# Optimization experiments

Measured on AMD Instinct MI355X. Metric: run time of the kernel, lower is better.

## Reference

```python
import jax, jax.numpy as jnp
import numpy as np

H = 1024        # hidden_size
NH = 16         # num_attention_heads
HD = H // NH    # attention_head_size = 64
EPS = 1e-12


def setup_inputs() -> dict:
    key = jax.random.key(0)
    ks = jax.random.split(key, 12)
    B, S = 2, 2048
    s = 0.02
    return {
        "hidden_states": jax.random.normal(ks[0], (B, S, H), jnp.float32),
        "attention_mask": jnp.zeros((B, 1, 1, S), jnp.float32),
        "Wq": jax.random.normal(ks[1], (H, H), jnp.float32) * s,
        "bq": jnp.zeros((H,), jnp.float32),
        "Wk": jax.random.normal(ks[2], (H, H), jnp.float32) * s,
        "bk": jnp.zeros((H,), jnp.float32),
        "Wv": jax.random.normal(ks[3], (H, H), jnp.float32) * s,
        "bv": jnp.zeros((H,), jnp.float32),
        "Wd": jax.random.normal(ks[4], (H, H), jnp.float32) * s,
        "bd": jnp.zeros((H,), jnp.float32),
        "ln_gamma": jnp.ones((H,), jnp.float32),
        "ln_beta": jnp.zeros((H,), jnp.float32),
    }


def _split_heads(x):
    # [B,S,H] -> [B,NH,S,HD]
    B, S, _ = x.shape
    return x.reshape(B, S, NH, HD).transpose(0, 2, 1, 3)


def reference(hidden_states, attention_mask, Wq, bq, Wk, bk, Wv, bv, Wd, bd, ln_gamma, ln_beta):
    q = _split_heads(hidden_states @ Wq.T + bq)
    k = _split_heads(hidden_states @ Wk.T + bk)
    v = _split_heads(hidden_states @ Wv.T + bv)

    scores = jnp.einsum("bhqd,bhkd->bhqk", q, k) / jnp.sqrt(jnp.float32(HD))
    scores = scores + attention_mask
    probs = jax.nn.softmax(scores, axis=-1)  # attention dropout p=0

    ctx = jnp.einsum("bhqk,bhkd->bhqd", probs, v)
    B, _, S, _ = ctx.shape
    ctx = ctx.transpose(0, 2, 1, 3).reshape(B, S, H)

    proj = ctx @ Wd.T + bd  # output dropout p=0
    x = hidden_states + proj
    mu = jnp.mean(x, axis=-1, keepdims=True)
    var = jnp.mean(jnp.square(x - mu), axis=-1, keepdims=True)
    out = (x - mu) * jax.lax.rsqrt(var + EPS) * ln_gamma + ln_beta
    return out
```

## Files before the change

kernel.cpp:

```cpp
#include <hip/hip_runtime.h>

typedef unsigned short u16;
typedef __attribute__((ext_vector_type(4))) unsigned short u16x4;
typedef __attribute__((ext_vector_type(8))) unsigned short u16x8;
typedef __attribute__((ext_vector_type(8))) __bf16 bf16x8;
typedef __attribute__((ext_vector_type(4))) float f32x4;

#define S_LEN 2048
#define HDIM 1024
#define NHEAD 16
#define HD 64
#define MTOK 4096
#define QKV_STRIDE 4194304
#define LOG2E 1.44269504089f
#define QKSCL (0.125f * 1.44269504089f)

__device__ __forceinline__ float bf2f(u16 h) {
    unsigned u = ((unsigned)h) << 16;
    return __builtin_bit_cast(float, u);
}
__device__ __forceinline__ u16 f2bf(float f) {
    return __builtin_bit_cast(u16, (__bf16)f);
}
__device__ __forceinline__ bf16x8 as_bf16(u16x8 u) {
    union { u16x8 a; bf16x8 b; } c; c.a = u; return c.b;
}
__device__ __forceinline__ void gld_lds16(const u16* g, u16* l) {
    __builtin_amdgcn_global_load_lds((const __attribute__((address_space(1))) u16*)g,
                                     (__attribute__((address_space(3))) u16*)l, 16, 0, 0);
}

__device__ __forceinline__ void cast4(const float* __restrict__ s, u16* __restrict__ d, int i) {
    f32x4 v = *(const f32x4*)(s + (size_t)i * 4);
    u16x4 o;
    o[0] = f2bf(v[0]); o[1] = f2bf(v[1]); o[2] = f2bf(v[2]); o[3] = f2bf(v[3]);
    *(u16x4*)(d + (size_t)i * 4) = o;
}

__global__ __launch_bounds__(256) void prep(const float* __restrict__ hs,
                                            const float* __restrict__ Wq, const float* __restrict__ Wk,
                                            const float* __restrict__ Wv, const float* __restrict__ Wd,
                                            const float* __restrict__ bq, const float* __restrict__ bk,
                                            const float* __restrict__ bv,
                                            u16* __restrict__ hsb, u16* __restrict__ wqkvb,
                                            u16* __restrict__ wdb, float* __restrict__ b3) {
    int bid = blockIdx.x, tid = threadIdx.x;
    if (bid < 4096) {
        cast4(hs, hsb, bid * 256 + tid);
    } else if (bid < 5120) {
        cast4(Wq, wqkvb, (bid - 4096) * 256 + tid);
    } else if (bid < 6144) {
        cast4(Wk, wqkvb + HDIM * HDIM, (bid - 5120) * 256 + tid);
    } else if (bid < 7168) {
        cast4(Wv, wqkvb + 2 * HDIM * HDIM, (bid - 6144) * 256 + tid);
    } else if (bid < 8192) {
        cast4(Wd, wdb, (bid - 7168) * 256 + tid);
    } else {
        int i = (bid - 8192) * 256 + tid;
        if (i < 3072) b3[i] = (i < 1024) ? bq[i] : (i < 2048) ? bk[i - 1024] : bv[i - 2048];
    }
}

template <int MODE>
__global__ __launch_bounds__(256, 3) void gemm_bt(const u16* __restrict__ A, const u16* __restrict__ Bw,
                                                  const float* __restrict__ bias,
                                                  u16* __restrict__ outb, u16* __restrict__ vtout,
                                                  float* __restrict__ outf,
                                                  int Md, int Nd, int Kd) {
    __shared__ alignas(16) u16 As[2][128 * 32];
    __shared__ alignas(16) u16 Bs[2][128 * 32];
    const int tid = threadIdx.x;
    const int wave = tid >> 6, lane = tid & 63;
    const int l15 = lane & 15, l4 = lane >> 4;
    const int m0 = blockIdx.y * 128, n0 = blockIdx.x * 128;
    const int wm = wave >> 1, wn = wave & 1;

    const int cc0 = wave * 2;
    const int srow = lane >> 2;
    const int sco = (lane & 3) * 8;

    f32x4 acc[4][4];
#pragma unroll
    for (int i = 0; i < 4; i++)
#pragma unroll
        for (int j = 0; j < 4; j++) acc[i][j] = (f32x4){0.f, 0.f, 0.f, 0.f};

    auto STAGE = [&](int k0, int buf) {
#pragma unroll
        for (int i = 0; i < 2; i++) {
            int cc = cc0 + i;
            int row = cc * 16 + srow;
            gld_lds16(A + (size_t)(m0 + row) * Kd + k0 + sco, &As[buf][cc * 512]);
            gld_lds16(Bw + (size_t)(n0 + row) * Kd + k0 + sco, &Bs[buf][cc * 512]);
        }
    };

    const int nt = Kd >> 5;
    STAGE(0, 0);
    for (int t = 0; t < nt; ++t) {
        __builtin_amdgcn_s_barrier();
        if (t + 1 < nt) {
            STAGE((t + 1) << 5, (t + 1) & 1);
            asm volatile("s_waitcnt vmcnt(4)" ::: "memory");
        } else {
            asm volatile("s_waitcnt vmcnt(0)" ::: "memory");
        }
        __builtin_amdgcn_s_barrier();
        const u16* as = &As[t & 1][0];
        const u16* bs = &Bs[t & 1][0];
        bf16x8 af[4], bf[4];
#pragma unroll
        for (int x = 0; x < 4; x++) {
            af[x] = as_bf16(*(const u16x8*)&as[(wm * 64 + x * 16 + l15) * 32 + l4 * 8]);
            bf[x] = as_bf16(*(const u16x8*)&bs[(wn * 64 + x * 16 + l15) * 32 + l4 * 8]);
        }
        __builtin_amdgcn_s_setprio(1);
#pragma unroll
        for (int mi = 0; mi < 4; mi++)
#pragma unroll
            for (int nj = 0; nj < 4; nj++)
                acc[mi][nj] = __builtin_amdgcn_mfma_f32_16x16x32_bf16(af[mi], bf[nj], acc[mi][nj], 0, 0, 0);
        __builtin_amdgcn_s_setprio(0);
    }

#pragma unroll
    for (int mi = 0; mi < 4; mi++) {
#pragma unroll
        for (int nj = 0; nj < 4; nj++) {
            int coln = n0 + wn * 64 + nj * 16 + l15;
            float bv_ = bias[coln];
            int rowb = m0 + wm * 64 + mi * 16 + l4 * 4;
            if (MODE == 0) {
                int which = coln >> 10, nn = coln & 1023;
                int hh = nn >> 6, dd = nn & 63;
                int bb = rowb >> 11, ss = rowb & 2047;
                if (which < 2) {
#pragma unroll
                    for (int r = 0; r < 4; r++)
                        outb[(size_t)which * QKV_STRIDE + ((size_t)((bb << 4) + hh) * S_LEN + ss + r) * HD + dd] =
                            f2bf(acc[mi][nj][r] + bv_);
                } else {
                    u16x4 o;
#pragma unroll
                    for (int r = 0; r < 4; r++) o[r] = f2bf(acc[mi][nj][r] + bv_);
                    *(u16x4*)(vtout + ((size_t)((bb << 4) + hh) * HD + dd) * S_LEN + ss) = o;
                }
            } else {
#pragma unroll
                for (int r = 0; r < 4; r++)
                    outf[(size_t)(rowb + r) * Nd + coln] = acc[mi][nj][r] + bv_;
            }
        }
    }
}

__global__ __launch_bounds__(512, 6) void flash_attn5(const u16* __restrict__ qkv,
                                                      const u16* __restrict__ vt,
                                                      const float* __restrict__ amask,
                                                      u16* __restrict__ ctx) {
    __shared__ alignas(16) u16 Kb[2][4096];
    __shared__ alignas(16) u16 Vb[2][4096];
    __shared__ alignas(16) u16 Pl[8][1024];
    __shared__ u16 Mlb[2048];

    const int tid = threadIdx.x;
    const int wave = tid >> 6, lane = tid & 63;
    const int l15 = lane & 15, l4 = lane >> 4;
    const int lid = blockIdx.x;
    const int idx = lid >> 3;
    const int bh = (lid & 7) * 4 + (idx >> 4);
    const int qx = idx & 15;
    const int b = bh >> 4, h = bh & 15;
    const int qr0 = qx * 128 + wave * 16;

    const u16* qh = qkv + (size_t)bh * (S_LEN * HD);
    const u16* kh = qh + QKV_STRIDE;
    const u16* vth = vt + (size_t)bh * (S_LEN * HD);
    u16* pw = &Pl[wave][0];

    {
        f32x4 m = *(const f32x4*)(amask + (size_t)b * S_LEN + tid * 4);
        u16x4 mm;
#pragma unroll
        for (int j = 0; j < 4; j++) mm[j] = f2bf(m[j] * LOG2E);
        *(u16x4*)&Mlb[tid * 4] = mm;
    }

    bf16x8 qf[2];
#pragma unroll
    for (int ks = 0; ks < 2; ks++)
        qf[ks] = as_bf16(*(const u16x8*)(qh + (size_t)(qr0 + l15) * HD + ks * 32 + l4 * 8));

    __syncthreads();

    const int srow = lane >> 3;
    const int schunk = (lane & 7) ^ srow;
    const int krow = wave * 8 + srow;
    const u16* ksrc = kh + (size_t)krow * HD + schunk * 8;
    const u16* vsrc = vth + (size_t)krow * S_LEN + schunk * 8;

    f32x4 acc_o[4];
    float l_run = 0.f;
#pragma unroll
    for (int x = 0; x < 4; x++) acc_o[x] = (f32x4){0.f, 0.f, 0.f, 0.f};

    auto STAGE = [&](int T, int buf) {
        gld_lds16(ksrc + (size_t)T * 64 * HD, &Kb[buf][wave * 512]);
        gld_lds16(vsrc + T * 64, &Vb[buf][wave * 512]);
    };

    auto tile = [&](int t, int buf) {
        const u16* kb = &Kb[buf][0];
        const u16* vb = &Vb[buf][0];
        f32x4 accs[4];
#pragma unroll
        for (int nj = 0; nj < 4; nj++) accs[nj] = (f32x4){0.f, 0.f, 0.f, 0.f};
        __builtin_amdgcn_s_setprio(1);
#pragma unroll
        for (int ks = 0; ks < 2; ks++) {
            bf16x8 kf[4];
#pragma unroll
            for (int nj = 0; nj < 4; nj++) {
                int n = nj * 16 + l15;
                kf[nj] = as_bf16(*(const u16x8*)&kb[n * 64 + ((ks * 32 + l4 * 8) ^ ((n & 7) << 3))]);
            }
#pragma unroll
            for (int nj = 0; nj < 4; nj++)
                accs[nj] = __builtin_amdgcn_mfma_f32_16x16x32_bf16(kf[nj], qf[ks], accs[nj], 0, 0, 0);
        }
        __builtin_amdgcn_s_setprio(0);
        const int kv0 = t * 64;
        const int rsw = (l15 & 7) << 3;
#pragma unroll
        for (int nj = 0; nj < 4; nj++) {
            u16x4 mraw = *(const u16x4*)&Mlb[kv0 + nj * 16 + l4 * 4];
            u16x4 o;
#pragma unroll
            for (int r = 0; r < 4; r++) {
                float p = __builtin_amdgcn_exp2f(accs[nj][r] * QKSCL + bf2f(mraw[r]));
                l_run += p;
                o[r] = f2bf(p);
            }
            *(u16x4*)&pw[l15 * 64 + ((nj * 16 + l4 * 4) ^ rsw)] = o;
        }
        __builtin_amdgcn_s_setprio(1);
#pragma unroll
        for (int ks = 0; ks < 2; ks++) {
            int kvoff = ks * 32 + l4 * 8;
            bf16x8 pf = as_bf16(*(const u16x8*)&pw[l15 * 64 + (kvoff ^ rsw)]);
            bf16x8 vf[4];
#pragma unroll
            for (int dj = 0; dj < 4; dj++) {
                int d = dj * 16 + l15;
                vf[dj] = as_bf16(*(const u16x8*)&vb[d * 64 + (kvoff ^ ((d & 7) << 3))]);
            }
#pragma unroll
            for (int dj = 0; dj < 4; dj++)
                acc_o[dj] = __builtin_amdgcn_mfma_f32_16x16x32_bf16(vf[dj], pf, acc_o[dj], 0, 0, 0);
        }
        __builtin_amdgcn_s_setprio(0);
    };

    STAGE(0, 0);
    for (int t = 0; t < 32; ++t) {
        __builtin_amdgcn_s_barrier();
        if (t + 1 < 32) {
            STAGE(t + 1, (t + 1) & 1);
            asm volatile("s_waitcnt vmcnt(2)" ::: "memory");
        } else {
            asm volatile("s_waitcnt vmcnt(0)" ::: "memory");
        }
        __builtin_amdgcn_s_barrier();
        tile(t, t & 1);
    }

    float l = l_run;
    l += __shfl_xor(l, 16);
    l += __shfl_xor(l, 32);
    float inv = 1.0f / l;
    u16* cp = ctx + ((size_t)b * S_LEN + qr0 + l15) * HDIM + h * HD + l4 * 4;
#pragma unroll
    for (int dj = 0; dj < 4; dj++) {
        u16x4 o;
#pragma unroll
        for (int r = 0; r < 4; r++) o[r] = f2bf(acc_o[dj][r] * inv);
        *(u16x4*)(cp + dj * 16) = o;
    }
}

__global__ __launch_bounds__(256) void resid_ln(const float* __restrict__ hs, const float* __restrict__ proj,
                                                const float* __restrict__ g, const float* __restrict__ be,
                                                float* __restrict__ out) {
    int row = blockIdx.x, tid = threadIdx.x;
    int base = row * HDIM + tid * 4;
    f32x4 a = *(const f32x4*)(hs + base);
    f32x4 p = *(const f32x4*)(proj + base);
    f32x4 x = a + p;
    float s = x[0] + x[1] + x[2] + x[3];
    float sq = x[0] * x[0] + x[1] * x[1] + x[2] * x[2] + x[3] * x[3];
#pragma unroll
    for (int m = 1; m < 64; m <<= 1) {
        s += __shfl_xor(s, m);
        sq += __shfl_xor(sq, m);
    }
    __shared__ float red[8];
    int wave = tid >> 6, lane = tid & 63;
    if (lane == 0) { red[wave] = s; red[4 + wave] = sq; }
    __syncthreads();
    s = red[0] + red[1] + red[2] + red[3];
    sq = red[4] + red[5] + red[6] + red[7];
    float mean = s * (1.0f / 1024.0f);
    float var = sq * (1.0f / 1024.0f) - mean * mean;
    float rstd = rsqrtf(fmaxf(var, 0.f) + 1e-12f);
    f32x4 gg = *(const f32x4*)(g + tid * 4);
    f32x4 bb = *(const f32x4*)(be + tid * 4);
    f32x4 o;
#pragma unroll
    for (int j = 0; j < 4; j++) o[j] = (x[j] - mean) * rstd * gg[j] + bb[j];
    *(f32x4*)(out + base) = o;
}

extern "C" void kernel_launch(void* const* d_in, const int* in_sizes, int n_in,
                              void* d_out, int out_size, void* d_ws, size_t ws_size,
                              hipStream_t stream) {
    const float* hs    = (const float*)d_in[0];
    const float* amask = (const float*)d_in[1];
    const float* Wq    = (const float*)d_in[2];
    const float* bq    = (const float*)d_in[3];
    const float* Wk    = (const float*)d_in[4];
    const float* bk    = (const float*)d_in[5];
    const float* Wv    = (const float*)d_in[6];
    const float* bv    = (const float*)d_in[7];
    const float* Wd    = (const float*)d_in[8];
    const float* bd    = (const float*)d_in[9];
    const float* gamma = (const float*)d_in[10];
    const float* beta  = (const float*)d_in[11];

    char* ws = (char*)d_ws;
    u16*   hsb   = (u16*)(ws);
    u16*   Wqkvb = (u16*)(ws + ((size_t)8 << 20));
    u16*   Wdb   = (u16*)(ws + ((size_t)14 << 20));
    u16*   qkv   = (u16*)(ws + ((size_t)16 << 20));
    u16*   vt    = qkv + 2 * (size_t)QKV_STRIDE;
    u16*   ctx   = (u16*)(ws + ((size_t)40 << 20));
    float* proj  = (float*)(ws + ((size_t)48 << 20));
    float* b3    = (float*)(ws + ((size_t)64 << 20));

    prep<<<8204, 256, 0, stream>>>(hs, Wq, Wk, Wv, Wd, bq, bk, bv, hsb, Wqkvb, Wdb, b3);

    gemm_bt<0><<<dim3(24, 32), 256, 0, stream>>>(hsb, Wqkvb, b3, qkv, vt, nullptr, MTOK, 3072, HDIM);

    flash_attn5<<<512, 512, 0, stream>>>(qkv, vt, amask, ctx);

    gemm_bt<1><<<dim3(8, 32), 256, 0, stream>>>(ctx, Wdb, bd, nullptr, nullptr, proj, MTOK, HDIM, HDIM);

    resid_ln<<<MTOK, 256, 0, stream>>>(hs, proj, gamma, beta, (float*)d_out);
}
```

Baseline: 128.4 us.

## Rework attention with 32x32 MFMA, in-register P via permlane, split-KV wave groups

The flash attention kernel switches from 16x16x32 to 32x32x16 bf16 MFMAs, with each wave handling 32 query rows. The probability tile now stays in registers: a permlane32 swap rearranges it into the B-operand layout instead of a round trip through LDS. The 8 waves form two groups that process alternating KV tiles, and their partial outputs and row sums are combined through shared memory at the end. The mask is kept in fp32, and the occupancy hint drops from 6 to 4 in exchange for larger register tiles and 72KB of LDS.

```diff
diff --git a/kernel.cpp b/kernel.cpp
--- a/kernel.cpp
+++ b/kernel.cpp
@@ -1,10 +1,13 @@
 #include <hip/hip_runtime.h>
 
 typedef unsigned short u16;
+typedef unsigned int u32;
 typedef __attribute__((ext_vector_type(4))) unsigned short u16x4;
 typedef __attribute__((ext_vector_type(8))) unsigned short u16x8;
 typedef __attribute__((ext_vector_type(8))) __bf16 bf16x8;
 typedef __attribute__((ext_vector_type(4))) float f32x4;
+typedef __attribute__((ext_vector_type(16))) float f32x16;
+typedef __attribute__((ext_vector_type(2))) int i32x2;
 
 #define S_LEN 2048
 #define HDIM 1024
@@ -28,6 +31,20 @@
 __device__ __forceinline__ void gld_lds16(const u16* g, u16* l) {
     __builtin_amdgcn_global_load_lds((const __attribute__((address_space(1))) u16*)g,
                                      (__attribute__((address_space(3))) u16*)l, 16, 0, 0);
+}
+
+__device__ __forceinline__ void pl32swap(u32& a, u32& b) {
+#if __has_builtin(__builtin_amdgcn_permlane32_swap)
+    i32x2 r = __builtin_amdgcn_permlane32_swap((int)a, (int)b, false, false);
+    a = (u32)r[0]; b = (u32)r[1];
+#else
+    u32 as = (u32)__shfl_xor((int)a, 32);
+    u32 bs = (u32)__shfl_xor((int)b, 32);
+    bool hi = (threadIdx.x & 32) != 0;
+    u32 na = hi ? bs : a;
+    u32 nb = hi ? b : as;
+    a = na; b = nb;
+#endif
 }
 
 __device__ __forceinline__ void cast4(const float* __restrict__ s, u16* __restrict__ d, int i) {
@@ -154,119 +171,133 @@
     }
 }
 
-__global__ __launch_bounds__(512, 6) void flash_attn5(const u16* __restrict__ qkv,
+__global__ __launch_bounds__(512, 4) void flash_attn6(const u16* __restrict__ qkv,
                                                       const u16* __restrict__ vt,
                                                       const float* __restrict__ amask,
                                                       u16* __restrict__ ctx) {
-    __shared__ alignas(16) u16 Kb[2][4096];
-    __shared__ alignas(16) u16 Vb[2][4096];
-    __shared__ alignas(16) u16 Pl[8][1024];
-    __shared__ u16 Mlb[2048];
+    __shared__ alignas(16) char smem[73728];
 
     const int tid = threadIdx.x;
     const int wave = tid >> 6, lane = tid & 63;
-    const int l15 = lane & 15, l4 = lane >> 4;
+    const int l31 = lane & 31;
+    const int hi = lane >> 5;
+    const int hi4 = hi * 4;
+    const int ws = wave & 3;
+    const int g = wave >> 2;
+
     const int lid = blockIdx.x;
     const int idx = lid >> 3;
     const int bh = (lid & 7) * 4 + (idx >> 4);
     const int qx = idx & 15;
     const int b = bh >> 4, h = bh & 15;
-    const int qr0 = qx * 128 + wave * 16;
+    const int qr0 = qx * 128 + ws * 32;
 
     const u16* qh = qkv + (size_t)bh * (S_LEN * HD);
     const u16* kh = qh + QKV_STRIDE;
     const u16* vth = vt + (size_t)bh * (S_LEN * HD);
-    u16* pw = &Pl[wave][0];
+
+    u16* kbase = (u16*)(smem + g * 32768);
+    u16* vbase = kbase + 8192;
+    float* Ml = (float*)(smem + 65536);
 
     {
         f32x4 m = *(const f32x4*)(amask + (size_t)b * S_LEN + tid * 4);
-        u16x4 mm;
-#pragma unroll
-        for (int j = 0; j < 4; j++) mm[j] = f2bf(m[j] * LOG2E);
-        *(u16x4*)&Mlb[tid * 4] = mm;
-    }
-
-    bf16x8 qf[2];
-#pragma unroll
-    for (int ks = 0; ks < 2; ks++)
-        qf[ks] = as_bf16(*(const u16x8*)(qh + (size_t)(qr0 + l15) * HD + ks * 32 + l4 * 8));
+#pragma unroll
+        for (int j = 0; j < 4; j++) m[j] *= LOG2E;
+        *(f32x4*)&Ml[tid * 4] = m;
+    }
+
+    bf16x8 qf[4];
+#pragma unroll
+    for (int s = 0; s < 4; ++s)
+        qf[s] = as_bf16(*(const u16x8*)(qh + (size_t)(qr0 + l31) * HD + s * 16 + hi * 8));
 
     __syncthreads();
 
     const int srow = lane >> 3;
     const int schunk = (lane & 7) ^ srow;
-    const int krow = wave * 8 + srow;
-    const u16* ksrc = kh + (size_t)krow * HD + schunk * 8;
-    const u16* vsrc = vth + (size_t)krow * S_LEN + schunk * 8;
-
-    f32x4 acc_o[4];
+    const u16* kss = kh + (size_t)(ws * 16 + srow) * HD + schunk * 8;
+    const u16* vss = vth + (size_t)(ws * 16 + srow) * S_LEN + schunk * 8;
+
+    f32x16 oacc[2];
+#pragma unroll
+    for (int d = 0; d < 2; ++d)
+#pragma unroll
+        for (int i = 0; i < 16; ++i) oacc[d][i] = 0.f;
     float l_run = 0.f;
-#pragma unroll
-    for (int x = 0; x < 4; x++) acc_o[x] = (f32x4){0.f, 0.f, 0.f, 0.f};
-
-    auto STAGE = [&](int T, int buf) {
-        gld_lds16(ksrc + (size_t)T * 64 * HD, &Kb[buf][wave * 512]);
-        gld_lds16(vsrc + T * 64, &Vb[buf][wave * 512]);
+
+    auto STAGE = [&](int tloc, int buf) {
+        const int kv0 = ((tloc << 1) + g) << 6;
+        const u16* ks = kss + (size_t)kv0 * HD;
+        const u16* vs = vss + kv0;
+        u16* kd = kbase + buf * 4096 + ws * 1024;
+        u16* vd = vbase + buf * 4096 + ws * 1024;
+        gld_lds16(ks, kd);
+        gld_lds16(ks + 8 * HD, kd + 512);
+        gld_lds16(vs, vd);
+        gld_lds16(vs + 8 * S_LEN, vd + 512);
     };
 
-    auto tile = [&](int t, int buf) {
-        const u16* kb = &Kb[buf][0];
-        const u16* vb = &Vb[buf][0];
-        f32x4 accs[4];
-#pragma unroll
-        for (int nj = 0; nj < 4; nj++) accs[nj] = (f32x4){0.f, 0.f, 0.f, 0.f};
-        __builtin_amdgcn_s_setprio(1);
-#pragma unroll
-        for (int ks = 0; ks < 2; ks++) {
-            bf16x8 kf[4];
-#pragma unroll
-            for (int nj = 0; nj < 4; nj++) {
-                int n = nj * 16 + l15;
-                kf[nj] = as_bf16(*(const u16x8*)&kb[n * 64 + ((ks * 32 + l4 * 8) ^ ((n & 7) << 3))]);
+    auto tile = [&](int tloc, int buf) {
+        const int kv0 = ((tloc << 1) + g) << 6;
+        const u16* kb = kbase + buf * 4096;
+        const u16* vb = vbase + buf * 4096;
+#pragma unroll
+        for (int sub = 0; sub < 2; ++sub) {
+            f32x16 accs;
+#pragma unroll
+            for (int i = 0; i < 16; ++i) accs[i] = 0.f;
+            const int kvrow = sub * 32 + l31;
+            const int ksw = (kvrow & 7) << 3;
+            __builtin_amdgcn_s_setprio(1);
+#pragma unroll
+            for (int s = 0; s < 4; ++s) {
+                bf16x8 kf = as_bf16(*(const u16x8*)&kb[kvrow * 64 + (((s * 2 + hi) << 3) ^ ksw)]);
+                accs = __builtin_amdgcn_mfma_f32_32x32x16_bf16(kf, qf[s], accs, 0, 0, 0);
             }
-#pragma unroll
-            for (int nj = 0; nj < 4; nj++)
-                accs[nj] = __builtin_amdgcn_mfma_f32_16x16x32_bf16(kf[nj], qf[ks], accs[nj], 0, 0, 0);
-        }
-        __builtin_amdgcn_s_setprio(0);
-        const int kv0 = t * 64;
-        const int rsw = (l15 & 7) << 3;
-#pragma unroll
-        for (int nj = 0; nj < 4; nj++) {
-            u16x4 mraw = *(const u16x4*)&Mlb[kv0 + nj * 16 + l4 * 4];
-            u16x4 o;
-#pragma unroll
-            for (int r = 0; r < 4; r++) {
-                float p = __builtin_amdgcn_exp2f(accs[nj][r] * QKSCL + bf2f(mraw[r]));
-                l_run += p;
-                o[r] = f2bf(p);
+            __builtin_amdgcn_s_setprio(0);
+            u32 pw_[8];
+#pragma unroll
+            for (int rg = 0; rg < 4; ++rg) {
+                f32x4 mk = *(const f32x4*)&Ml[kv0 + sub * 32 + rg * 8 + hi4];
+#pragma unroll
+                for (int r2 = 0; r2 < 2; ++r2) {
+                    float pa = __builtin_amdgcn_exp2f(accs[rg * 4 + r2 * 2] * QKSCL + mk[r2 * 2]);
+                    float pb = __builtin_amdgcn_exp2f(accs[rg * 4 + r2 * 2 + 1] * QKSCL + mk[r2 * 2 + 1]);
+                    l_run += pa + pb;
+                    pw_[rg * 2 + r2] = (u32)f2bf(pa) | ((u32)f2bf(pb) << 16);
+                }
             }
-            *(u16x4*)&pw[l15 * 64 + ((nj * 16 + l4 * 4) ^ rsw)] = o;
-        }
-        __builtin_amdgcn_s_setprio(1);
-#pragma unroll
-        for (int ks = 0; ks < 2; ks++) {
-            int kvoff = ks * 32 + l4 * 8;
-            bf16x8 pf = as_bf16(*(const u16x8*)&pw[l15 * 64 + (kvoff ^ rsw)]);
-            bf16x8 vf[4];
-#pragma unroll
-            for (int dj = 0; dj < 4; dj++) {
-                int d = dj * 16 + l15;
-                vf[dj] = as_bf16(*(const u16x8*)&vb[d * 64 + (kvoff ^ ((d & 7) << 3))]);
+            pl32swap(pw_[0], pw_[2]);
+            pl32swap(pw_[1], pw_[3]);
+            pl32swap(pw_[4], pw_[6]);
+            pl32swap(pw_[5], pw_[7]);
+            union { u32 w[4]; u16x8 v; } f0, f1;
+            f0.w[0] = pw_[0]; f0.w[1] = pw_[1]; f0.w[2] = pw_[2]; f0.w[3] = pw_[3];
+            f1.w[0] = pw_[4]; f1.w[1] = pw_[5]; f1.w[2] = pw_[6]; f1.w[3] = pw_[7];
+            bf16x8 pf0 = as_bf16(f0.v), pf1 = as_bf16(f1.v);
+            __builtin_amdgcn_s_setprio(1);
+#pragma unroll
+            for (int dsub = 0; dsub < 2; ++dsub) {
+                const int drow = dsub * 32 + l31;
+                const int dsw = (drow & 7) << 3;
+                const int c0 = (sub * 4 + hi) << 3;
+                const int c1 = ((sub * 2 + 1) * 2 + hi) << 3;
+                bf16x8 vf0 = as_bf16(*(const u16x8*)&vb[drow * 64 + (c0 ^ dsw)]);
+                oacc[dsub] = __builtin_amdgcn_mfma_f32_32x32x16_bf16(vf0, pf0, oacc[dsub], 0, 0, 0);
+                bf16x8 vf1 = as_bf16(*(const u16x8*)&vb[drow * 64 + (c1 ^ dsw)]);
+                oacc[dsub] = __builtin_amdgcn_mfma_f32_32x32x16_bf16(vf1, pf1, oacc[dsub], 0, 0, 0);
             }
-#pragma unroll
-            for (int dj = 0; dj < 4; dj++)
-                acc_o[dj] = __builtin_amdgcn_mfma_f32_16x16x32_bf16(vf[dj], pf, acc_o[dj], 0, 0, 0);
-        }
-        __builtin_amdgcn_s_setprio(0);
+            __builtin_amdgcn_s_setprio(0);
+        }
     };
 
     STAGE(0, 0);
-    for (int t = 0; t < 32; ++t) {
+    for (int t = 0; t < 16; ++t) {
         __builtin_amdgcn_s_barrier();
-        if (t + 1 < 32) {
+        if (t + 1 < 16) {
             STAGE(t + 1, (t + 1) & 1);
-            asm volatile("s_waitcnt vmcnt(2)" ::: "memory");
+            asm volatile("s_waitcnt vmcnt(4)" ::: "memory");
         } else {
             asm volatile("s_waitcnt vmcnt(0)" ::: "memory");
         }
@@ -274,17 +305,40 @@
         tile(t, t & 1);
     }
 
-    float l = l_run;
-    l += __shfl_xor(l, 16);
-    l += __shfl_xor(l, 32);
-    float inv = 1.0f / l;
-    u16* cp = ctx + ((size_t)b * S_LEN + qr0 + l15) * HDIM + h * HD + l4 * 4;
-#pragma unroll
-    for (int dj = 0; dj < 4; dj++) {
-        u16x4 o;
-#pragma unroll
-        for (int r = 0; r < 4; r++) o[r] = f2bf(acc_o[dj][r] * inv);
-        *(u16x4*)(cp + dj * 16) = o;
+    float* Oex = (float*)smem;
+    float* lsum = (float*)(smem + 32768);
+    __syncthreads();
+    if (g == 1) {
+#pragma unroll
+        for (int dsub = 0; dsub < 2; ++dsub)
+#pragma unroll
+            for (int rg = 0; rg < 4; ++rg)
+#pragma unroll
+                for (int rr = 0; rr < 4; ++rr) {
+                    int d = dsub * 32 + hi4 + rr + 8 * rg;
+                    Oex[ws * 2048 + d * 32 + l31] = oacc[dsub][rg * 4 + rr];
+                }
+        float lB = l_run + __shfl_xor(l_run, 32);
+        if (lane < 32) lsum[ws * 32 + lane] = lB;
+    }
+    __syncthreads();
+    if (g == 0) {
+        float lt = l_run + __shfl_xor(l_run, 32) + lsum[ws * 32 + l31];
+        float inv = 1.0f / lt;
+        u16* cp = ctx + ((size_t)b * S_LEN + qr0 + l31) * HDIM + h * HD;
+#pragma unroll
+        for (int dsub = 0; dsub < 2; ++dsub)
+#pragma unroll
+            for (int rg = 0; rg < 4; ++rg) {
+                u16x4 o;
+#pragma unroll
+                for (int rr = 0; rr < 4; ++rr) {
+                    int d = dsub * 32 + hi4 + rr + 8 * rg;
+                    float v = oacc[dsub][rg * 4 + rr] + Oex[ws * 2048 + d * 32 + l31];
+                    o[rr] = f2bf(v * inv);
+                }
+                *(u16x4*)(cp + dsub * 32 + hi4 + 8 * rg) = o;
+            }
     }
 }
 
@@ -350,7 +404,7 @@
 
     gemm_bt<0><<<dim3(24, 32), 256, 0, stream>>>(hsb, Wqkvb, b3, qkv, vt, nullptr, MTOK, 3072, HDIM);
 
-    flash_attn5<<<512, 512, 0, stream>>>(qkv, vt, amask, ctx);
+    flash_attn6<<<512, 512, 0, stream>>>(qkv, vt, amask, ctx);
 
     gemm_bt<1><<<dim3(8, 32), 256, 0, stream>>>(ctx, Wdb, bd, nullptr, nullptr, proj, MTOK, HDIM, HDIM);
 
```

After: 129.2 us. Within noise of the previous version (+0.6%).

## Triple-buffer K/V tiles in attention and store projection output as bf16

Applied to the files above, without the earlier changes.

The attention kernel moves from double to triple buffering of K/V tiles. It prefetches two tiles ahead and drops one barrier per iteration, to hide more global-memory latency. This raises LDS use per block, and the occupancy hint drops from 6 to 4. Separately, the output-projection GEMM now writes bf16 instead of fp32, halving its write traffic and the read traffic in the residual+LayerNorm kernel, at some cost in precision of the projection before the residual add.

```diff
diff --git a/kernel.cpp b/kernel.cpp
--- a/kernel.cpp
+++ b/kernel.cpp
@@ -1,6 +1,7 @@
 #include <hip/hip_runtime.h>
 
 typedef unsigned short u16;
+typedef unsigned int u32;
 typedef __attribute__((ext_vector_type(4))) unsigned short u16x4;
 typedef __attribute__((ext_vector_type(8))) unsigned short u16x8;
 typedef __attribute__((ext_vector_type(8))) __bf16 bf16x8;
@@ -61,14 +62,12 @@
     }
 }
 
-template <int MODE>
-__global__ __launch_bounds__(256, 3) void gemm_bt(const u16* __restrict__ A, const u16* __restrict__ Bw,
-                                                  const float* __restrict__ bias,
-                                                  u16* __restrict__ outb, u16* __restrict__ vtout,
-                                                  float* __restrict__ outf,
-                                                  int Md, int Nd, int Kd) {
+__global__ __launch_bounds__(256, 3) void gemm_qkv(const u16* __restrict__ A, const u16* __restrict__ Bw,
+                                                   const float* __restrict__ bias,
+                                                   u16* __restrict__ outb, u16* __restrict__ vtout) {
     __shared__ alignas(16) u16 As[2][128 * 32];
     __shared__ alignas(16) u16 Bs[2][128 * 32];
+    const int Kd = 1024;
     const int tid = threadIdx.x;
     const int wave = tid >> 6, lane = tid & 63;
     const int l15 = lane & 15, l4 = lane >> 4;
@@ -130,36 +129,103 @@
             int coln = n0 + wn * 64 + nj * 16 + l15;
             float bv_ = bias[coln];
             int rowb = m0 + wm * 64 + mi * 16 + l4 * 4;
-            if (MODE == 0) {
-                int which = coln >> 10, nn = coln & 1023;
-                int hh = nn >> 6, dd = nn & 63;
-                int bb = rowb >> 11, ss = rowb & 2047;
-                if (which < 2) {
-#pragma unroll
-                    for (int r = 0; r < 4; r++)
-                        outb[(size_t)which * QKV_STRIDE + ((size_t)((bb << 4) + hh) * S_LEN + ss + r) * HD + dd] =
-                            f2bf(acc[mi][nj][r] + bv_);
-                } else {
-                    u16x4 o;
-#pragma unroll
-                    for (int r = 0; r < 4; r++) o[r] = f2bf(acc[mi][nj][r] + bv_);
-                    *(u16x4*)(vtout + ((size_t)((bb << 4) + hh) * HD + dd) * S_LEN + ss) = o;
-                }
+            int which = coln >> 10, nn = coln & 1023;
+            int hh = nn >> 6, dd = nn & 63;
+            int bb = rowb >> 11, ss = rowb & 2047;
+            if (which < 2) {
+#pragma unroll
+                for (int r = 0; r < 4; r++)
+                    outb[(size_t)which * QKV_STRIDE + ((size_t)((bb << 4) + hh) * S_LEN + ss + r) * HD + dd] =
+                        f2bf(acc[mi][nj][r] + bv_);
             } else {
-#pragma unroll
-                for (int r = 0; r < 4; r++)
-                    outf[(size_t)(rowb + r) * Nd + coln] = acc[mi][nj][r] + bv_;
+                u16x4 o;
+#pragma unroll
+                for (int r = 0; r < 4; r++) o[r] = f2bf(acc[mi][nj][r] + bv_);
+                *(u16x4*)(vtout + ((size_t)((bb << 4) + hh) * HD + dd) * S_LEN + ss) = o;
             }
         }
     }
 }
 
-__global__ __launch_bounds__(512, 6) void flash_attn5(const u16* __restrict__ qkv,
+__global__ __launch_bounds__(256, 3) void gemm_proj(const u16* __restrict__ A, const u16* __restrict__ Bw,
+                                                    const float* __restrict__ bias,
+                                                    u16* __restrict__ outb, int Nd, int Kd) {
+    __shared__ alignas(16) u16 As[2][128 * 32];
+    __shared__ alignas(16) u16 Bs[2][128 * 32];
+    const int tid = threadIdx.x;
+    const int wave = tid >> 6, lane = tid & 63;
+    const int l15 = lane & 15, l4 = lane >> 4;
+    const int m0 = blockIdx.y * 128, n0 = blockIdx.x * 128;
+    const int wm = wave >> 1, wn = wave & 1;
+
+    const int cc0 = wave * 2;
+    const int srow = lane >> 2;
+    const int sco = (lane & 3) * 8;
+
+    f32x4 acc[4][4];
+#pragma unroll
+    for (int i = 0; i < 4; i++)
+#pragma unroll
+        for (int j = 0; j < 4; j++) acc[i][j] = (f32x4){0.f, 0.f, 0.f, 0.f};
+
+    auto STAGE = [&](int k0, int buf) {
+#pragma unroll
+        for (int i = 0; i < 2; i++) {
+            int cc = cc0 + i;
+            int row = cc * 16 + srow;
+            gld_lds16(A + (size_t)(m0 + row) * Kd + k0 + sco, &As[buf][cc * 512]);
+            gld_lds16(Bw + (size_t)(n0 + row) * Kd + k0 + sco, &Bs[buf][cc * 512]);
+        }
+    };
+
+    const int nt = Kd >> 5;
+    STAGE(0, 0);
+    for (int t = 0; t < nt; ++t) {
+        __builtin_amdgcn_s_barrier();
+        if (t + 1 < nt) {
+            STAGE((t + 1) << 5, (t + 1) & 1);
+            asm volatile("s_waitcnt vmcnt(4)" ::: "memory");
+        } else {
+            asm volatile("s_waitcnt vmcnt(0)" ::: "memory");
+        }
+        __builtin_amdgcn_s_barrier();
+        const u16* as = &As[t & 1][0];
+        const u16* bs = &Bs[t & 1][0];
+        bf16x8 af[4], bf[4];
+#pragma unroll
+        for (int x = 0; x < 4; x++) {
+            af[x] = as_bf16(*(const u16x8*)&as[(wm * 64 + x * 16 + l15) * 32 + l4 * 8]);
+            bf[x] = as_bf16(*(const u16x8*)&bs[(wn * 64 + x * 16 + l15) * 32 + l4 * 8]);
+        }
+        __builtin_amdgcn_s_setprio(1);
+#pragma unroll
+        for (int mi = 0; mi < 4; mi++)
+#pragma unroll
+            for (int nj = 0; nj < 4; nj++)
+                acc[mi][nj] = __builtin_amdgcn_mfma_f32_16x16x32_bf16(af[mi], bf[nj], acc[mi][nj], 0, 0, 0);
+        __builtin_amdgcn_s_setprio(0);
+    }
+
+#pragma unroll
+    for (int mi = 0; mi < 4; mi++) {
+#pragma unroll
+        for (int nj = 0; nj < 4; nj++) {
+            int coln = n0 + wn * 64 + nj * 16 + l15;
+            float bv_ = bias[coln];
+            int rowb = m0 + wm * 64 + mi * 16 + l4 * 4;
+#pragma unroll
+            for (int r = 0; r < 4; r++)
+                outb[(size_t)(rowb + r) * Nd + coln] = f2bf(acc[mi][nj][r] + bv_);
+        }
+    }
+}
+
+__global__ __launch_bounds__(512, 4) void flash_attn9(const u16* __restrict__ qkv,
                                                       const u16* __restrict__ vt,
                                                       const float* __restrict__ amask,
                                                       u16* __restrict__ ctx) {
-    __shared__ alignas(16) u16 Kb[2][4096];
-    __shared__ alignas(16) u16 Vb[2][4096];
+    __shared__ alignas(16) u16 Kb[3][4096];
+    __shared__ alignas(16) u16 Vb[3][4096];
     __shared__ alignas(16) u16 Pl[8][1024];
     __shared__ u16 Mlb[2048];
 
@@ -262,16 +328,16 @@
     };
 
     STAGE(0, 0);
+    STAGE(1, 1);
     for (int t = 0; t < 32; ++t) {
-        __builtin_amdgcn_s_barrier();
-        if (t + 1 < 32) {
-            STAGE(t + 1, (t + 1) & 1);
+        if (t < 31) {
             asm volatile("s_waitcnt vmcnt(2)" ::: "memory");
         } else {
             asm volatile("s_waitcnt vmcnt(0)" ::: "memory");
         }
         __builtin_amdgcn_s_barrier();
-        tile(t, t & 1);
+        if (t + 2 < 32) STAGE(t + 2, (t + 2) % 3);
+        tile(t, t % 3);
     }
 
     float l = l_run;
@@ -288,14 +354,16 @@
     }
 }
 
-__global__ __launch_bounds__(256) void resid_ln(const float* __restrict__ hs, const float* __restrict__ proj,
+__global__ __launch_bounds__(256) void resid_ln(const float* __restrict__ hs, const u16* __restrict__ proj,
                                                 const float* __restrict__ g, const float* __restrict__ be,
                                                 float* __restrict__ out) {
     int row = blockIdx.x, tid = threadIdx.x;
     int base = row * HDIM + tid * 4;
     f32x4 a = *(const f32x4*)(hs + base);
-    f32x4 p = *(const f32x4*)(proj + base);
-    f32x4 x = a + p;
+    u16x4 pb = *(const u16x4*)(proj + base);
+    f32x4 x;
+#pragma unroll
+    for (int j = 0; j < 4; j++) x[j] = a[j] + bf2f(pb[j]);
     float s = x[0] + x[1] + x[2] + x[3];
     float sq = x[0] * x[0] + x[1] * x[1] + x[2] * x[2] + x[3] * x[3];
 #pragma unroll
@@ -343,16 +411,16 @@
     u16*   qkv   = (u16*)(ws + ((size_t)16 << 20));
     u16*   vt    = qkv + 2 * (size_t)QKV_STRIDE;
     u16*   ctx   = (u16*)(ws + ((size_t)40 << 20));
-    float* proj  = (float*)(ws + ((size_t)48 << 20));
+    u16*   projb = (u16*)(ws + ((size_t)48 << 20));
     float* b3    = (float*)(ws + ((size_t)64 << 20));
 
     prep<<<8204, 256, 0, stream>>>(hs, Wq, Wk, Wv, Wd, bq, bk, bv, hsb, Wqkvb, Wdb, b3);
 
-    gemm_bt<0><<<dim3(24, 32), 256, 0, stream>>>(hsb, Wqkvb, b3, qkv, vt, nullptr, MTOK, 3072, HDIM);
-
-    flash_attn5<<<512, 512, 0, stream>>>(qkv, vt, amask, ctx);
-
-    gemm_bt<1><<<dim3(8, 32), 256, 0, stream>>>(ctx, Wdb, bd, nullptr, nullptr, proj, MTOK, HDIM, HDIM);
-
-    resid_ln<<<MTOK, 256, 0, stream>>>(hs, proj, gamma, beta, (float*)d_out);
-}
+    gemm_qkv<<<dim3(24, 32), 256, 0, stream>>>(hsb, Wqkvb, b3, qkv, vt);
+
+    flash_attn9<<<512, 512, 0, stream>>>(qkv, vt, amask, ctx);
+
+    gemm_proj<<<dim3(8, 32), 256, 0, stream>>>(ctx, Wdb, bd, projb, HDIM, HDIM);
+
+    resid_ln<<<MTOK, 256, 0, stream>>>(hs, projb, gamma, beta, (float*)d_out);
+}
```

Measured after the change: 127.0 us. Within noise of the previous version (-1.1%).
